# Performance work log

Hardware: AMD Instinct MI355X
Metric: run time of the kernel (lower is better)

The kernel has to match this reference:

```python
import jax, jax.numpy as jnp
import numpy as np

N_NODES = 50000
N_REL = 8
N_EDGES = 60000
F_IN = 128
UNITS = 128


def setup_inputs() -> dict:
    key = jax.random.key(0)
    ks = jax.random.split(key, 7)
    features = jax.random.normal(ks[0], (1, N_NODES, F_IN), dtype=jnp.float32)
    edge_src = jax.random.randint(ks[1], (N_REL, N_EDGES), 0, N_NODES, dtype=jnp.int32)
    edge_dst = jax.random.randint(ks[2], (N_REL, N_EDGES), 0, N_NODES, dtype=jnp.int32)
    edge_w = jax.random.uniform(ks[3], (N_REL, N_EDGES), dtype=jnp.float32)
    scale = 1.0 / np.sqrt(F_IN)
    self_kernel = jax.random.normal(ks[4], (F_IN, UNITS), dtype=jnp.float32) * scale
    rel_kernels = jax.random.normal(ks[5], (N_REL, F_IN, UNITS), dtype=jnp.float32) * scale
    bias = jnp.zeros((UNITS,), dtype=jnp.float32)
    return {"features": features, "edge_src": edge_src, "edge_dst": edge_dst,
            "edge_w": edge_w, "self_kernel": self_kernel,
            "rel_kernels": rel_kernels, "bias": bias}


def reference(features, edge_src, edge_dst, edge_w, self_kernel, rel_kernels, bias):
    # features: [1, N, F]; squeeze the batch dim like the original layer
    x = features[0]                                   # [N, F]
    out = x @ self_kernel                             # [N, U] self-loop term
    # per-relation feature transform: [R, N, U]
    hr = jnp.einsum('nf,rfu->rnu', x, rel_kernels)
    # sparse A_r @ hr via gather at src, weight, segment-sum into dst
    def per_rel(h, s, d, w):
        msg = h[s] * w[:, None]                       # [E, U]
        return jax.ops.segment_sum(msg, d, num_segments=N_NODES)
    agg = jax.vmap(per_rel)(hr, edge_src, edge_dst, edge_w)  # [R, N, U]
    out = out + agg.sum(axis=0) + bias
    out = jax.nn.relu(out)
    return out[None]                                  # [1, N, U]
```

## Files before the change

kernel.cpp:

```cpp
#include <hip/hip_runtime.h>
#include <hip/hip_bf16.h>

#define NN 50000
#define FF 128
#define UU 128
#define NREL 8
#define NE 60000
#define NKEY (NREL * NN)
#define NET (NREL * NE)

typedef __attribute__((ext_vector_type(8))) short bf16x8;
typedef __attribute__((ext_vector_type(4))) float f32x4;


__global__ __launch_bounds__(256) void prep_kernel(
    const float* __restrict__ X, const float* __restrict__ Wself,
    const float* __restrict__ Wrel, ushort* __restrict__ Xb,
    ushort* __restrict__ Wf, int* __restrict__ head)
{
    int i = blockIdx.x * 256 + threadIdx.x;
    if (i < NN * FF / 4) {
        float4 v = ((const float4*)X)[i];
        union { __hip_bfloat162 h[2]; uint2 u; } p;
        p.h[0] = __float22bfloat162_rn(make_float2(v.x, v.y));
        p.h[1] = __float22bfloat162_rn(make_float2(v.z, v.w));
        ((uint2*)Xb)[i] = p.u;
    }
    if (i < NKEY) head[i] = -1;
    if (i < 9 * FF * UU) {
        int m = i >> 14, k = (i >> 7) & 127, col = i & 127;
        int c = col >> 4, al = col & 15;
        int s = k >> 5, ag = (k >> 3) & 3, j = k & 7;
        float v = (m == 0) ? Wself[i] : Wrel[i - FF * UU];
        __hip_bfloat16 h = __float2bfloat16(v);
        Wf[((m * 8 + c) * 4 + s) * 512 + (ag * 16 + al) * 8 + j] = *(ushort*)&h;
    }
}


__global__ __launch_bounds__(256) void build_kernel(
    const int* __restrict__ esrc, const int* __restrict__ edst,
    const float* __restrict__ ew, int* __restrict__ head, int4* __restrict__ rec)
{
    int i = blockIdx.x * 256 + threadIdx.x;
    if (i < NET) {
        int key = (i / NE) * NN + edst[i];
        int prev = atomicExch(&head[key], i);
        rec[i] = make_int4(esrc[i], __float_as_int(ew[i]), prev, 0);
    }
}


#define AGG_WALK(e, r, ax, ay)                                              \
    while (e >= 0) {                                                        \
        float w = __int_as_float(r.y);                                      \
        uint x = *(const uint*)(Xb + (size_t)r.x * FF + 2 * l);             \
        e = r.z;                                                            \
        if (e >= 0) r = rec[e];                                             \
        ax = fmaf(__uint_as_float(x << 16), w, ax);                         \
        ay = fmaf(__uint_as_float(x & 0xffff0000u), w, ay);                 \
    }

__global__ __launch_bounds__(256) void agg_kernel(
    const ushort* __restrict__ Xb, const int* __restrict__ head,
    const int4* __restrict__ rec, ushort* __restrict__ Zb)
{
    const int k0 = ((blockIdx.x * 256 + threadIdx.x) >> 6) * 4;
    const int l = threadIdx.x & 63;

    float a0x = 0.f, a0y = 0.f, a1x = 0.f, a1y = 0.f;
    float a2x = 0.f, a2y = 0.f, a3x = 0.f, a3y = 0.f;

    const int4 hv = *(const int4*)&head[k0];
    int e0 = hv.x, e1 = hv.y, e2 = hv.z, e3 = hv.w;
    int4 r0, r1, r2, r3;
    if (e0 >= 0) r0 = rec[e0];
    if (e1 >= 0) r1 = rec[e1];
    if (e2 >= 0) r2 = rec[e2];
    if (e3 >= 0) r3 = rec[e3];

    AGG_WALK(e0, r0, a0x, a0y)
    AGG_WALK(e1, r1, a1x, a1y)
    AGG_WALK(e2, r2, a2x, a2y)
    AGG_WALK(e3, r3, a3x, a3y)

    __hip_bfloat162 h;
    h = __float22bfloat162_rn(make_float2(a0x, a0y));
    *(uint*)(Zb + (size_t)(k0 + 0) * FF + 2 * l) = *(uint*)&h;
    h = __float22bfloat162_rn(make_float2(a1x, a1y));
    *(uint*)(Zb + (size_t)(k0 + 1) * FF + 2 * l) = *(uint*)&h;
    h = __float22bfloat162_rn(make_float2(a2x, a2y));
    *(uint*)(Zb + (size_t)(k0 + 2) * FF + 2 * l) = *(uint*)&h;
    h = __float22bfloat162_rn(make_float2(a3x, a3y));
    *(uint*)(Zb + (size_t)(k0 + 3) * FF + 2 * l) = *(uint*)&h;
}


#define LOAD_A(AF, P)                                                        \
    _Pragma("unroll")                                                        \
    for (int s = 0; s < 4; ++s)                                              \
        AF[s] = *(const bf16x8*)((P) + s * 32 + ag * 8);

#define MFMA_BURST(AF)                                                       \
    _Pragma("unroll")                                                        \
    for (int c = 0; c < 8; ++c) {                                            \
        _Pragma("unroll")                                                    \
        for (int s = 0; s < 4; ++s) {                                        \
            bf16x8 bfr = *(const bf16x8*)&bsh[(c * 4 + s) * 64 + l];         \
            acc[c] = __builtin_amdgcn_mfma_f32_16x16x32_bf16(                \
                AF[s], bfr, acc[c], 0, 0, 0);                                \
        }                                                                    \
    }

__global__ __launch_bounds__(256, 3) void gemm_kernel(
    const ushort* __restrict__ Xb, const ushort* __restrict__ Zb,
    const ushort* __restrict__ Wf, const float* __restrict__ bias,
    float* __restrict__ out)
{
    __shared__ uint4 bsh[2048];
    const int t = threadIdx.x;
    const int wid = t >> 6;
    const int l = t & 63;
    const int gw0 = blockIdx.x * 4 + wid;
    const int gwid = (gw0 < NN / 16) ? gw0 : NN / 16 - 1;
    const int R0 = gwid * 16;
    const int al = l & 15;
    const int ag = l >> 4;

    const uint4* Wf4 = (const uint4*)Wf;

    f32x4 acc[8];
    #pragma unroll
    for (int c = 0; c < 8; ++c) acc[c] = (f32x4){0.f, 0.f, 0.f, 0.f};

    uint4 stg0 = Wf4[t +    0], stg1 = Wf4[t +  256];
    uint4 stg2 = Wf4[t +  512], stg3 = Wf4[t +  768];
    uint4 stg4 = Wf4[t + 1024], stg5 = Wf4[t + 1280];
    uint4 stg6 = Wf4[t + 1536], stg7 = Wf4[t + 1792];

    bf16x8 aA[4], aB[4];
    {
        const ushort* A0 = Xb + (size_t)(R0 + al) * FF;
        LOAD_A(aA, A0)
    }

    #pragma unroll
    for (int m = 0; m < 9; ++m) {
        __syncthreads();
        bsh[t +    0] = stg0; bsh[t +  256] = stg1;
        bsh[t +  512] = stg2; bsh[t +  768] = stg3;
        bsh[t + 1024] = stg4; bsh[t + 1280] = stg5;
        bsh[t + 1536] = stg6; bsh[t + 1792] = stg7;
        if (m < 8) {
            const uint4* Wn = Wf4 + (m + 1) * 2048;
            stg0 = Wn[t +    0]; stg1 = Wn[t +  256];
            stg2 = Wn[t +  512]; stg3 = Wn[t +  768];
            stg4 = Wn[t + 1024]; stg5 = Wn[t + 1280];
            stg6 = Wn[t + 1536]; stg7 = Wn[t + 1792];
        }
        if (m < 8) {
            const ushort* An = Zb + ((size_t)m * NN + R0 + al) * FF;
            if ((m & 1) == 0) { LOAD_A(aB, An) } else { LOAD_A(aA, An) }
        }
        __syncthreads();
        if ((m & 1) == 0) { MFMA_BURST(aA) } else { MFMA_BURST(aB) }
    }

    #pragma unroll
    for (int c = 0; c < 8; ++c) {
        int col = c * 16 + al;
        float b = bias[col];
        #pragma unroll
        for (int q = 0; q < 4; ++q) {
            int row = R0 + ag * 4 + q;
            out[(size_t)row * UU + col] = fmaxf(acc[c][q] + b, 0.f);
        }
    }
}


extern "C" void kernel_launch(void* const* d_in, const int* in_sizes, int n_in,
                              void* d_out, int out_size, void* d_ws, size_t ws_size,
                              hipStream_t stream) {
    const float* X     = (const float*)d_in[0];
    const int*   esrc  = (const int*)d_in[1];
    const int*   edst  = (const int*)d_in[2];
    const float* ew    = (const float*)d_in[3];
    const float* Wself = (const float*)d_in[4];
    const float* Wrel  = (const float*)d_in[5];
    const float* bias  = (const float*)d_in[6];
    float* out = (float*)d_out;

    ushort* Zb   = (ushort*)d_ws;
    ushort* Xb   = Zb + (size_t)NKEY * FF;
    ushort* Wf   = Xb + (size_t)NN * FF;
    int*    head = (int*)(Wf + 9 * FF * UU);
    int4*   rec  = (int4*)(head + NKEY);

    hipLaunchKernelGGL(prep_kernel,  dim3(NN * FF / 4 / 256), dim3(256), 0, stream,
                       X, Wself, Wrel, Xb, Wf, head);
    hipLaunchKernelGGL(build_kernel, dim3((NET + 255) / 256), dim3(256), 0, stream,
                       esrc, edst, ew, head, rec);
    hipLaunchKernelGGL(agg_kernel,   dim3(NKEY / 16), dim3(256), 0, stream,
                       Xb, head, rec, Zb);
    hipLaunchKernelGGL(gemm_kernel,  dim3((NN / 16 + 3) / 4), dim3(256), 0, stream,
                       Xb, Zb, Wf, bias, out);
}
```

Before: 127.1 us.

## Fuse prep and build kernels, memset head, load weights directly to LDS

```diff
diff --git a/kernel.cpp b/kernel.cpp
--- a/kernel.cpp
+++ b/kernel.cpp
@@ -13,10 +13,12 @@
 typedef __attribute__((ext_vector_type(4))) float f32x4;
 
 
-__global__ __launch_bounds__(256) void prep_kernel(
+__global__ __launch_bounds__(256) void prepbuild_kernel(
     const float* __restrict__ X, const float* __restrict__ Wself,
-    const float* __restrict__ Wrel, ushort* __restrict__ Xb,
-    ushort* __restrict__ Wf, int* __restrict__ head)
+    const float* __restrict__ Wrel, const int* __restrict__ esrc,
+    const int* __restrict__ edst, const float* __restrict__ ew,
+    ushort* __restrict__ Xb, ushort* __restrict__ Wf,
+    int* __restrict__ head, int4* __restrict__ rec)
 {
     int i = blockIdx.x * 256 + threadIdx.x;
     if (i < NN * FF / 4) {
@@ -26,7 +28,11 @@
         p.h[1] = __float22bfloat162_rn(make_float2(v.z, v.w));
         ((uint2*)Xb)[i] = p.u;
     }
-    if (i < NKEY) head[i] = -1;
+    if (i < NET) {
+        int key = (i / NE) * NN + edst[i];
+        int prev = atomicExch(&head[key], i);
+        rec[i] = make_int4(esrc[i], __float_as_int(ew[i]), prev, 0);
+    }
     if (i < 9 * FF * UU) {
         int m = i >> 14, k = (i >> 7) & 127, col = i & 127;
         int c = col >> 4, al = col & 15;
@@ -34,19 +40,6 @@
         float v = (m == 0) ? Wself[i] : Wrel[i - FF * UU];
         __hip_bfloat16 h = __float2bfloat16(v);
         Wf[((m * 8 + c) * 4 + s) * 512 + (ag * 16 + al) * 8 + j] = *(ushort*)&h;
-    }
-}
-
-
-__global__ __launch_bounds__(256) void build_kernel(
-    const int* __restrict__ esrc, const int* __restrict__ edst,
-    const float* __restrict__ ew, int* __restrict__ head, int4* __restrict__ rec)
-{
-    int i = blockIdx.x * 256 + threadIdx.x;
-    if (i < NET) {
-        int key = (i / NE) * NN + edst[i];
-        int prev = atomicExch(&head[key], i);
-        rec[i] = make_int4(esrc[i], __float_as_int(ew[i]), prev, 0);
     }
 }
 
@@ -96,6 +89,12 @@
 }
 
 
+__device__ __forceinline__ void gload_lds16(const uint4* g, uint4* l) {
+    __builtin_amdgcn_global_load_lds(
+        (const __attribute__((address_space(1))) void*)g,
+        (__attribute__((address_space(3))) void*)l, 16, 0, 0);
+}
+
 #define LOAD_A(AF, P)                                                        \
     _Pragma("unroll")                                                        \
     for (int s = 0; s < 4; ++s)                                              \
@@ -112,7 +111,7 @@
         }                                                                    \
     }
 
-__global__ __launch_bounds__(256, 3) void gemm_kernel(
+__global__ __launch_bounds__(256, 4) void gemm_kernel(
     const ushort* __restrict__ Xb, const ushort* __restrict__ Zb,
     const ushort* __restrict__ Wf, const float* __restrict__ bias,
     float* __restrict__ out)
@@ -133,11 +132,6 @@
     #pragma unroll
     for (int c = 0; c < 8; ++c) acc[c] = (f32x4){0.f, 0.f, 0.f, 0.f};
 
-    uint4 stg0 = Wf4[t +    0], stg1 = Wf4[t +  256];
-    uint4 stg2 = Wf4[t +  512], stg3 = Wf4[t +  768];
-    uint4 stg4 = Wf4[t + 1024], stg5 = Wf4[t + 1280];
-    uint4 stg6 = Wf4[t + 1536], stg7 = Wf4[t + 1792];
-
     bf16x8 aA[4], aB[4];
     {
         const ushort* A0 = Xb + (size_t)(R0 + al) * FF;
@@ -147,16 +141,12 @@
     #pragma unroll
     for (int m = 0; m < 9; ++m) {
         __syncthreads();
-        bsh[t +    0] = stg0; bsh[t +  256] = stg1;
-        bsh[t +  512] = stg2; bsh[t +  768] = stg3;
-        bsh[t + 1024] = stg4; bsh[t + 1280] = stg5;
-        bsh[t + 1536] = stg6; bsh[t + 1792] = stg7;
-        if (m < 8) {
-            const uint4* Wn = Wf4 + (m + 1) * 2048;
-            stg0 = Wn[t +    0]; stg1 = Wn[t +  256];
-            stg2 = Wn[t +  512]; stg3 = Wn[t +  768];
-            stg4 = Wn[t + 1024]; stg5 = Wn[t + 1280];
-            stg6 = Wn[t + 1536]; stg7 = Wn[t + 1792];
+        {
+            const uint4* Wm = Wf4 + m * 2048 + wid * 64 + l;
+            uint4* lb = &bsh[wid * 64];
+            #pragma unroll
+            for (int k = 0; k < 8; ++k)
+                gload_lds16(Wm + k * 256, lb + k * 256);
         }
         if (m < 8) {
             const ushort* An = Zb + ((size_t)m * NN + R0 + al) * FF;
@@ -197,12 +187,11 @@
     int*    head = (int*)(Wf + 9 * FF * UU);
     int4*   rec  = (int4*)(head + NKEY);
 
-    hipLaunchKernelGGL(prep_kernel,  dim3(NN * FF / 4 / 256), dim3(256), 0, stream,
-                       X, Wself, Wrel, Xb, Wf, head);
-    hipLaunchKernelGGL(build_kernel, dim3((NET + 255) / 256), dim3(256), 0, stream,
-                       esrc, edst, ew, head, rec);
-    hipLaunchKernelGGL(agg_kernel,   dim3(NKEY / 16), dim3(256), 0, stream,
+    hipMemsetAsync(head, 0xFF, NKEY * sizeof(int), stream);
+    hipLaunchKernelGGL(prepbuild_kernel, dim3(NN * FF / 4 / 256), dim3(256), 0, stream,
+                       X, Wself, Wrel, esrc, edst, ew, Xb, Wf, head, rec);
+    hipLaunchKernelGGL(agg_kernel,  dim3(NKEY / 16), dim3(256), 0, stream,
                        Xb, head, rec, Zb);
-    hipLaunchKernelGGL(gemm_kernel,  dim3((NN / 16 + 3) / 4), dim3(256), 0, stream,
+    hipLaunchKernelGGL(gemm_kernel, dim3((NN / 16 + 3) / 4), dim3(256), 0, stream,
                        Xb, Zb, Wf, bias, out);
 }
```

Measured after the change: 126.9 us. No clear change (-0.1%).
